# Optimization experiments

Hardware: AMD Instinct MI355X
Metric: run time of the kernel (lower is better)

## Reference

```python
import jax, jax.numpy as jnp
import numpy as np

# Tree/model constants (perfect binary plan tree in heap layout)
B = 256          # batch of plan trees
DEPTH = 10       # tree depth -> 512 leaves, 511 internal nodes
F = 64           # per-node feature dim
H = 512          # hidden_dim
DV = 64          # data_vec_dim
OUT = 1 + DV     # unit output: latency + data vector
N_LEAF = 2 ** (DEPTH - 1)
N_INT = N_LEAF - 1
N_NODE = N_INT + N_LEAF


def _mlp(x, w0, b0, w1, b1, w2, b2, wo, bo):
    # GenericUnit: num_layers=3 ReLU linears + linear head to OUT
    h = jax.nn.relu(x @ w0 + b0)
    h = jax.nn.relu(h @ w1 + b1)
    h = jax.nn.relu(h @ w2 + b2)
    return h @ wo + bo


def setup_inputs() -> dict:
    key = jax.random.key(0)
    ks = jax.random.split(key, 18)

    def lin(k, fan_in, shape):
        return (jax.random.normal(k, shape, jnp.float32) / np.sqrt(fan_in)).astype(jnp.float32)

    IIN = F + 2 * OUT  # internal unit input: features + two child outputs
    return {
        'leaf_feats': jax.random.normal(ks[0], (B, N_LEAF, F), jnp.float32),
        'internal_feats': jax.random.normal(ks[1], (B, N_INT, F), jnp.float32),
        # leaf unit (0 children)
        'lw0': lin(ks[2], F, (F, H)),   'lb0': jnp.zeros((H,), jnp.float32),
        'lw1': lin(ks[3], H, (H, H)),   'lb1': jnp.zeros((H,), jnp.float32),
        'lw2': lin(ks[4], H, (H, H)),   'lb2': jnp.zeros((H,), jnp.float32),
        'lwo': lin(ks[5], H, (H, OUT)), 'lbo': jnp.zeros((OUT,), jnp.float32),
        # internal unit (2 children)
        'iw0': lin(ks[6], IIN, (IIN, H)), 'ib0': jnp.zeros((H,), jnp.float32),
        'iw1': lin(ks[7], H, (H, H)),     'ib1': jnp.zeros((H,), jnp.float32),
        'iw2': lin(ks[8], H, (H, H)),     'ib2': jnp.zeros((H,), jnp.float32),
        'iwo': lin(ks[9], H, (H, OUT)),   'ibo': jnp.zeros((OUT,), jnp.float32),
    }


def reference(leaf_feats, internal_feats,
              lw0, lb0, lw1, lb1, lw2, lb2, lwo, lbo,
              iw0, ib0, iw1, ib1, iw2, ib2, iwo, ibo):
    # outputs buffer over all nodes, heap layout: internal [0, N_INT), leaves [N_INT, N_NODE)
    out = jnp.zeros((B, N_NODE, OUT), leaf_feats.dtype)
    out = out.at[:, N_INT:].set(_mlp(leaf_feats, lw0, lb0, lw1, lb1, lw2, lb2, lwo, lbo))
    # level-synchronous bottom-up over internal levels (fixed structural loop)
    for l in range(DEPTH - 2, -1, -1):
        s, e = 2 ** l - 1, 2 ** (l + 1) - 1
        left = out[:, 2 * s + 1:2 * e:2]        # children 2i+1
        right = out[:, 2 * s + 2:2 * e + 1:2]   # children 2i+2
        x = jnp.concatenate([internal_feats[:, s:e], left, right], axis=-1)
        out = out.at[:, s:e].set(_mlp(x, iw0, ib0, iw1, ib1, iw2, ib2, iwo, ibo))
    # root latency per tree: output[:, 0] of the root node
    return out[:, 0, 0]
```

## Files before the change

### kernel.cpp

```cpp
#include <hip/hip_runtime.h>
#include <cstdint>
#include <cstddef>
#include <type_traits>

#define OUT_DIM    65
#define TREE_STRIDE 66
#define N_NODE     1023
#define N_INTN     511

typedef _Float16 f16;
typedef _Float16 f16x8 __attribute__((ext_vector_type(8)));
typedef _Float16 f16x4 __attribute__((ext_vector_type(4)));
typedef float    f32x4 __attribute__((ext_vector_type(4)));

template<int V> using ic = std::integral_constant<int, V>;

#define MFMA(a, b, c) __builtin_amdgcn_mfma_f32_16x16x32_f16((a), (b), (c), 0, 0, 0)

template<int VM, int LG>
__device__ __forceinline__ void waitcnt_t() {
  asm volatile("s_waitcnt vmcnt(%0) lgkmcnt(%1)" :: "n"(VM), "n"(LG) : "memory");
}

template<int MT>
__device__ __forceinline__ void storeH_fn(f16* __restrict__ H, f32x4 (&acc)[MT][4],
                                          const float* __restrict__ bias,
                                          int wcb, int quad, int l16) {
#pragma unroll
  for (int mt = 0; mt < MT; mt++) {
#pragma unroll
    for (int nt = 0; nt < 4; nt++) {
      const int c0 = wcb + nt * 16 + quad * 4;
      const float4 bv = *(const float4*)(bias + c0);
      f16x4 hv;
      float v0 = acc[mt][nt][0] + bv.x; hv[0] = (f16)(v0 > 0.f ? v0 : 0.f);
      float v1 = acc[mt][nt][1] + bv.y; hv[1] = (f16)(v1 > 0.f ? v1 : 0.f);
      float v2 = acc[mt][nt][2] + bv.z; hv[2] = (f16)(v2 > 0.f ? v2 : 0.f);
      float v3 = acc[mt][nt][3] + bv.w; hv[3] = (f16)(v3 > 0.f ? v3 : 0.f);
      const int row = mt * 16 + l16;
      *(f16x4*)&H[row * 512 + (((c0 >> 3) ^ l16) << 3) + (quad & 1) * 4] = hv;
    }
  }
}

template<int NC, int MT, int NT, int BD, int AD, bool AGLOB, bool SWAP,
         typename GetB, typename GetA>
__device__ __forceinline__ void kloop(GetB getB, GetA getA, f32x4 (&acc)[MT][NT])
{
  f16x8 bs[BD][NT];
  f16x8 as[AD][MT];
#pragma unroll
  for (int c = 0; c < BD - 1 && c < NC; c++)
#pragma unroll
    for (int nt = 0; nt < NT; nt++) bs[c][nt] = getB(c, nt);
#pragma unroll
  for (int c = 0; c < AD - 1 && c < NC; c++)
#pragma unroll
    for (int mt = 0; mt < MT; mt++) as[c][mt] = getA(c, mt);

  auto lp = [&](auto&& self, auto Cc) -> void {
    constexpr int C = decltype(Cc)::value;
    if constexpr (C < NC) {
      if constexpr (C + BD - 1 < NC) {
#pragma unroll
        for (int nt = 0; nt < NT; nt++) bs[(C + BD - 1) % BD][nt] = getB(C + BD - 1, nt);
      }
      if constexpr (C + AD - 1 < NC) {
#pragma unroll
        for (int mt = 0; mt < MT; mt++) as[(C + AD - 1) % AD][mt] = getA(C + AD - 1, mt);
      }
      constexpr int BOUT = (BD - 1) < (NC - 1 - C) ? (BD - 1) : (NC - 1 - C);
      constexpr int AOUT = (AD - 1) < (NC - 1 - C) ? (AD - 1) : (NC - 1 - C);
      if constexpr (AGLOB) waitcnt_t<0, 0>();
      else                 waitcnt_t<NT * BOUT, MT * AOUT>();
      __builtin_amdgcn_s_setprio(1);
#pragma unroll
      for (int mt = 0; mt < MT; mt++)
#pragma unroll
        for (int nt = 0; nt < NT; nt++)
          acc[mt][nt] = SWAP ? MFMA(bs[C % BD][nt], as[C % AD][mt], acc[mt][nt])
                             : MFMA(as[C % AD][mt], bs[C % BD][nt], acc[mt][nt]);
      __builtin_amdgcn_s_setprio(0);
      self(self, ic<C + 1>{});
    }
  };
  lp(lp, ic<0>{});
}

template<int K, bool AGLOB, typename GetA>
__device__ __forceinline__ void run_layer(
    const f16* __restrict__ Wt, const float* __restrict__ bias,
    f16* __restrict__ H, int wave, int lane, int quad, int l16, GetA getA)
{
  constexpr int NC = K / 32;
  const int wcb = wave * 64;
  const f16* bbase = Wt + (long)(wave * 4) * 512 + lane * 8;
  auto getB = [&](int c, int nt) -> f16x8 {
    return *(const f16x8*)(bbase + (long)(c * 32 + nt) * 512);
  };
  f32x4 acc[4][4];
#pragma unroll
  for (int i = 0; i < 4; i++)
#pragma unroll
    for (int j = 0; j < 4; j++) acc[i][j] = f32x4{0.f, 0.f, 0.f, 0.f};

  kloop<NC, 4, 4, 4, 2, AGLOB, true>(getB, getA, acc);

  __syncthreads();
  storeH_fn<4>(H, acc, bias, wcb, quad, l16);
  __syncthreads();
}

__global__ __launch_bounds__(512, 2) void fused_mlp(
    const float* __restrict__ feats,
    const f16* __restrict__ w0t, const float* __restrict__ b0,
    const f16* __restrict__ w1t, const float* __restrict__ b1,
    const f16* __restrict__ w2t, const float* __restrict__ b2,
    const f16* __restrict__ wot, const float* __restrict__ bo,
    f16* __restrict__ tree, float* __restrict__ dOut, int lvl, int leaf)
{
  extern __shared__ f16 S[];
  f16* H = S;
  f16* X = S;

  const int tid  = threadIdx.x;
  const int wave = tid >> 6;
  const int lane = tid & 63;
  const int quad = lane >> 4;
  const int l16  = lane & 15;
  const long rowBase = (long)blockIdx.x * 64;

  if (!leaf) {
    for (int i = tid; i < 4096; i += 512) {
      int r = i >> 6, cc = i & 63;
      long rg = rowBase + r;
      long bbr = rg >> lvl;
      long ii = rg - (bbr << lvl);
      long nn = (1L << lvl) - 1 + ii;
      X[r * 232 + cc] = (f16)feats[(bbr * N_INTN + nn) * 64 + cc];
    }
    for (int i = tid; i < 4224; i += 512) {
      int r = i / 66, c = i - r * 66;
      long rg = rowBase + r;
      long bbr = rg >> lvl;
      long ii = rg - (bbr << lvl);
      long nn = (1L << lvl) - 1 + ii;
      const uint32_t* src = (const uint32_t*)(tree + (bbr * N_NODE + 2 * nn + 1) * TREE_STRIDE);
      *(uint32_t*)(X + r * 232 + 64 + 2 * c) = src[c];
    }
    for (int i = tid; i < 1792; i += 512) {
      int r = i / 28, cc = i - r * 28;
      X[r * 232 + 196 + cc] = (f16)0.f;
    }
    __syncthreads();
  }

  if (leaf) {
    auto gA = [&](int c, int mt) -> f16x8 {
      const float4* p = (const float4*)(feats + (rowBase + mt * 16 + l16) * 64 + c * 32 + quad * 8);
      float4 u0 = p[0], u1 = p[1];
      f16x8 a;
      a[0] = (f16)u0.x; a[1] = (f16)u0.y; a[2] = (f16)u0.z; a[3] = (f16)u0.w;
      a[4] = (f16)u1.x; a[5] = (f16)u1.y; a[6] = (f16)u1.z; a[7] = (f16)u1.w;
      return a;
    };
    run_layer<64, true>(w0t, b0, H, wave, lane, quad, l16, gA);
  } else {
    auto gA = [&](int c, int mt) -> f16x8 {
      int row = mt * 16 + l16;
      return *(const f16x8*)&X[row * 232 + c * 32 + quad * 8];
    };
    run_layer<224, false>(w0t, b0, H, wave, lane, quad, l16, gA);
  }

  auto getAH = [&](int c, int mt) -> f16x8 {
    int row = mt * 16 + l16;
    return *(const f16x8*)&H[row * 512 + ((((c * 4 + quad) ^ l16) << 3))];
  };
  run_layer<512, false>(w1t, b1, H, wave, lane, quad, l16, getAH);
  run_layer<512, false>(w2t, b2, H, wave, lane, quad, l16, getAH);

  if (wave < 4) {
    const f16* obase = wot + lane * 8;
    auto gB = [&](int c, int nt) -> f16x8 {
      return *(const f16x8*)(obase + (long)(c * 5 + nt) * 512);
    };
    const int orow = wave * 16 + l16;
    auto gA = [&](int c, int mt) -> f16x8 {
      return *(const f16x8*)&H[orow * 512 + ((((c * 4 + quad) ^ l16) << 3))];
    };
    f32x4 oacc[1][5];
#pragma unroll
    for (int i = 0; i < 5; i++) oacc[0][i] = f32x4{0.f, 0.f, 0.f, 0.f};

    kloop<16, 1, 5, 3, 2, false, false>(gB, gA, oacc);

#pragma unroll
    for (int nt = 0; nt < 5; nt++)
#pragma unroll
      for (int r = 0; r < 4; r++) {
        int col = nt * 16 + l16;
        long rg = rowBase + wave * 16 + quad * 4 + r;
        long b2_ = rg >> lvl;
        long ii  = rg - (b2_ << lvl);
        long node = (1L << lvl) - 1 + ii;
        if (col < OUT_DIM) {
          float v = oacc[0][nt][r] + bo[col];
          tree[(b2_ * N_NODE + node) * TREE_STRIDE + col] = (f16)v;
          if (lvl == 0 && col == 0) dOut[rg] = v;
        } else if (col == OUT_DIM) {
          tree[(b2_ * N_NODE + node) * TREE_STRIDE + col] = (f16)0.f;
        }
      }
  }
}

struct WSeg { const float* W; f16* Wt; int K, N, NB, hole, start; };
struct WPack { WSeg s[8]; int total; };

__global__ void wcast_all(WPack p) {
  int idx = blockIdx.x * 256 + threadIdx.x;
  if (idx >= p.total) return;
  int si = 0;
#pragma unroll
  for (int i = 1; i < 8; i++) if (idx >= p.s[i].start) si = i;
  WSeg sg = p.s[si];
  int e = idx - sg.start;
  int j = e & 7, lane = (e >> 3) & 63, q = e >> 9;
  int cb = q % sg.NB, c = q / sg.NB;
  int col = cb * 16 + (lane & 15);
  int k = c * 32 + (lane >> 4) * 8 + j;
  int srck = (k < sg.hole) ? k : k - 1;
  float v = (k != sg.hole && srck < sg.K && col < sg.N)
                ? sg.W[(long)srck * sg.N + col] : 0.f;
  sg.Wt[e] = (f16)v;
}

extern "C" void kernel_launch(void* const* d_in, const int* in_sizes, int n_in,
                              void* d_out, int out_size, void* d_ws, size_t ws_size,
                              hipStream_t stream) {
  const float* leaf_feats     = (const float*)d_in[0];
  const float* internal_feats = (const float*)d_in[1];
  const float* lw0 = (const float*)d_in[2];
  const float* lb0 = (const float*)d_in[3];
  const float* lw1 = (const float*)d_in[4];
  const float* lb1 = (const float*)d_in[5];
  const float* lw2 = (const float*)d_in[6];
  const float* lb2 = (const float*)d_in[7];
  const float* lwo = (const float*)d_in[8];
  const float* lbo = (const float*)d_in[9];
  const float* iw0 = (const float*)d_in[10];
  const float* ib0 = (const float*)d_in[11];
  const float* iw1 = (const float*)d_in[12];
  const float* ib1 = (const float*)d_in[13];
  const float* iw2 = (const float*)d_in[14];
  const float* ib2 = (const float*)d_in[15];
  const float* iwo = (const float*)d_in[16];
  const float* ibo = (const float*)d_in[17];
  float* dOut = (float*)d_out;

  char* ws = (char*)d_ws;
  size_t off = 0;
  auto alloc = [&](size_t bytes) -> void* {
    void* p = ws + off;
    off += (bytes + 255) & ~(size_t)255;
    return p;
  };

  f16* lw0t = (f16*)alloc((size_t)64  * 512 * 2);
  f16* lw1t = (f16*)alloc((size_t)512 * 512 * 2);
  f16* lw2t = (f16*)alloc((size_t)512 * 512 * 2);
  f16* lwot = (f16*)alloc((size_t)512 * 80  * 2);
  f16* iw0t = (f16*)alloc((size_t)224 * 512 * 2);
  f16* iw1t = (f16*)alloc((size_t)512 * 512 * 2);
  f16* iw2t = (f16*)alloc((size_t)512 * 512 * 2);
  f16* iwot = (f16*)alloc((size_t)512 * 80  * 2);
  f16* tree = (f16*)alloc((size_t)256 * N_NODE * TREE_STRIDE * 2);

  const int NOHOLE = 1 << 30;
  WPack p;
  int cum = 0;
  auto seg = [&](int i, const float* W, f16* Wt, int K, int N, int Kpad, int NB, int hole) {
    p.s[i] = {W, Wt, K, N, NB, hole, cum};
    cum += Kpad * NB * 16;
  };
  seg(0, lw0, lw0t, 64, 512, 64, 32, NOHOLE);
  seg(1, lw1, lw1t, 512, 512, 512, 32, NOHOLE);
  seg(2, lw2, lw2t, 512, 512, 512, 32, NOHOLE);
  seg(3, lwo, lwot, 512, 65, 512, 5, NOHOLE);
  seg(4, iw0, iw0t, 194, 512, 224, 32, 129);
  seg(5, iw1, iw1t, 512, 512, 512, 32, NOHOLE);
  seg(6, iw2, iw2t, 512, 512, 512, 32, NOHOLE);
  seg(7, iwo, iwot, 512, 65, 512, 5, NOHOLE);
  p.total = cum;
  wcast_all<<<dim3((cum + 255) / 256), dim3(256), 0, stream>>>(p);

  static bool attrSet = false;
  if (!attrSet) {
    hipFuncSetAttribute(reinterpret_cast<const void*>(fused_mlp),
                        hipFuncAttributeMaxDynamicSharedMemorySize, 65536);
    attrSet = true;
  }

  const size_t shmem = 65536;

  fused_mlp<<<dim3(2048), dim3(512), shmem, stream>>>(
      leaf_feats, lw0t, lb0, lw1t, lb1, lw2t, lb2, lwot, lbo, tree, dOut, 9, 1);

  for (int l = 8; l >= 0; l--) {
    fused_mlp<<<dim3(4u << l), dim3(512), shmem, stream>>>(
        internal_feats, iw0t, ib0, iw1t, ib1, iw2t, ib2, iwot, ibo, tree, dOut, l, 0);
  }

  (void)in_sizes; (void)n_in; (void)out_size; (void)ws_size;
}
```

Baseline: 662.2 us.

## Double rows per block to 128 so each weight tile serves more rows

Each block now processes 128 rows instead of 64, with 8 M-tiles per wave, which halves the number of blocks and doubles reuse of each loaded weight fragment. The leaf input is staged through shared memory rather than read directly from global, LDS grows to 128KB, and the software pipelining depth is reduced to make room for the larger accumulators. All 8 waves now compute the output head. The cost is more accumulator registers and LDS per block, which lowers occupancy, and fewer blocks at the small upper tree levels.

```diff
diff --git a/kernel.cpp b/kernel.cpp
--- a/kernel.cpp
+++ b/kernel.cpp
@@ -43,7 +43,7 @@
   }
 }
 
-template<int NC, int MT, int NT, int BD, int AD, bool AGLOB, bool SWAP,
+template<int NC, int MT, int NT, int BD, int AD, bool SWAP,
          typename GetB, typename GetA>
 __device__ __forceinline__ void kloop(GetB getB, GetA getA, f32x4 (&acc)[MT][NT])
 {
@@ -71,8 +71,7 @@
       }
       constexpr int BOUT = (BD - 1) < (NC - 1 - C) ? (BD - 1) : (NC - 1 - C);
       constexpr int AOUT = (AD - 1) < (NC - 1 - C) ? (AD - 1) : (NC - 1 - C);
-      if constexpr (AGLOB) waitcnt_t<0, 0>();
-      else                 waitcnt_t<NT * BOUT, MT * AOUT>();
+      waitcnt_t<NT * BOUT, MT * AOUT>();
       __builtin_amdgcn_s_setprio(1);
 #pragma unroll
       for (int mt = 0; mt < MT; mt++)
@@ -87,7 +86,7 @@
   lp(lp, ic<0>{});
 }
 
-template<int K, bool AGLOB, typename GetA>
+template<int K, typename GetA>
 __device__ __forceinline__ void run_layer(
     const f16* __restrict__ Wt, const float* __restrict__ bias,
     f16* __restrict__ H, int wave, int lane, int quad, int l16, GetA getA)
@@ -98,16 +97,16 @@
   auto getB = [&](int c, int nt) -> f16x8 {
     return *(const f16x8*)(bbase + (long)(c * 32 + nt) * 512);
   };
-  f32x4 acc[4][4];
-#pragma unroll
-  for (int i = 0; i < 4; i++)
+  f32x4 acc[8][4];
+#pragma unroll
+  for (int i = 0; i < 8; i++)
 #pragma unroll
     for (int j = 0; j < 4; j++) acc[i][j] = f32x4{0.f, 0.f, 0.f, 0.f};
 
-  kloop<NC, 4, 4, 4, 2, AGLOB, true>(getB, getA, acc);
+  kloop<NC, 8, 4, 2, 1, true>(getB, getA, acc);
 
   __syncthreads();
-  storeH_fn<4>(H, acc, bias, wcb, quad, l16);
+  storeH_fn<8>(H, acc, bias, wcb, quad, l16);
   __syncthreads();
 }
 
@@ -128,10 +127,16 @@
   const int lane = tid & 63;
   const int quad = lane >> 4;
   const int l16  = lane & 15;
-  const long rowBase = (long)blockIdx.x * 64;
-
-  if (!leaf) {
-    for (int i = tid; i < 4096; i += 512) {
+  const long rowBase = (long)blockIdx.x * 128;
+
+  if (leaf) {
+    for (int i = tid; i < 8192; i += 512) {
+      int r = i >> 6, cc = i & 63;
+      X[r * 72 + cc] = (f16)feats[(rowBase + r) * 64 + cc];
+    }
+    __syncthreads();
+  } else {
+    for (int i = tid; i < 8192; i += 512) {
       int r = i >> 6, cc = i & 63;
       long rg = rowBase + r;
       long bbr = rg >> lvl;
@@ -139,7 +144,7 @@
       long nn = (1L << lvl) - 1 + ii;
       X[r * 232 + cc] = (f16)feats[(bbr * N_INTN + nn) * 64 + cc];
     }
-    for (int i = tid; i < 4224; i += 512) {
+    for (int i = tid; i < 8448; i += 512) {
       int r = i / 66, c = i - r * 66;
       long rg = rowBase + r;
       long bbr = rg >> lvl;
@@ -148,7 +153,7 @@
       const uint32_t* src = (const uint32_t*)(tree + (bbr * N_NODE + 2 * nn + 1) * TREE_STRIDE);
       *(uint32_t*)(X + r * 232 + 64 + 2 * c) = src[c];
     }
-    for (int i = tid; i < 1792; i += 512) {
+    for (int i = tid; i < 3584; i += 512) {
       int r = i / 28, cc = i - r * 28;
       X[r * 232 + 196 + cc] = (f16)0.f;
     }
@@ -157,30 +162,26 @@
 
   if (leaf) {
     auto gA = [&](int c, int mt) -> f16x8 {
-      const float4* p = (const float4*)(feats + (rowBase + mt * 16 + l16) * 64 + c * 32 + quad * 8);
-      float4 u0 = p[0], u1 = p[1];
-      f16x8 a;
-      a[0] = (f16)u0.x; a[1] = (f16)u0.y; a[2] = (f16)u0.z; a[3] = (f16)u0.w;
-      a[4] = (f16)u1.x; a[5] = (f16)u1.y; a[6] = (f16)u1.z; a[7] = (f16)u1.w;
-      return a;
+      int row = mt * 16 + l16;
+      return *(const f16x8*)&X[row * 72 + c * 32 + quad * 8];
     };
-    run_layer<64, true>(w0t, b0, H, wave, lane, quad, l16, gA);
+    run_layer<64>(w0t, b0, H, wave, lane, quad, l16, gA);
   } else {
     auto gA = [&](int c, int mt) -> f16x8 {
       int row = mt * 16 + l16;
       return *(const f16x8*)&X[row * 232 + c * 32 + quad * 8];
     };
-    run_layer<224, false>(w0t, b0, H, wave, lane, quad, l16, gA);
+    run_layer<224>(w0t, b0, H, wave, lane, quad, l16, gA);
   }
 
   auto getAH = [&](int c, int mt) -> f16x8 {
     int row = mt * 16 + l16;
     return *(const f16x8*)&H[row * 512 + ((((c * 4 + quad) ^ l16) << 3))];
   };
-  run_layer<512, false>(w1t, b1, H, wave, lane, quad, l16, getAH);
-  run_layer<512, false>(w2t, b2, H, wave, lane, quad, l16, getAH);
-
-  if (wave < 4) {
+  run_layer<512>(w1t, b1, H, wave, lane, quad, l16, getAH);
+  run_layer<512>(w2t, b2, H, wave, lane, quad, l16, getAH);
+
+  {
     const f16* obase = wot + lane * 8;
     auto gB = [&](int c, int nt) -> f16x8 {
       return *(const f16x8*)(obase + (long)(c * 5 + nt) * 512);
@@ -193,7 +194,7 @@
 #pragma unroll
     for (int i = 0; i < 5; i++) oacc[0][i] = f32x4{0.f, 0.f, 0.f, 0.f};
 
-    kloop<16, 1, 5, 3, 2, false, false>(gB, gA, oacc);
+    kloop<16, 1, 5, 2, 1, false>(gB, gA, oacc);
 
 #pragma unroll
     for (int nt = 0; nt < 5; nt++)
@@ -298,17 +299,17 @@
   static bool attrSet = false;
   if (!attrSet) {
     hipFuncSetAttribute(reinterpret_cast<const void*>(fused_mlp),
-                        hipFuncAttributeMaxDynamicSharedMemorySize, 65536);
+                        hipFuncAttributeMaxDynamicSharedMemorySize, 131072);
     attrSet = true;
   }
 
-  const size_t shmem = 65536;
-
-  fused_mlp<<<dim3(2048), dim3(512), shmem, stream>>>(
+  const size_t shmem = 131072;
+
+  fused_mlp<<<dim3(1024), dim3(512), shmem, stream>>>(
       leaf_feats, lw0t, lb0, lw1t, lb1, lw2t, lb2, lwot, lbo, tree, dOut, 9, 1);
 
   for (int l = 8; l >= 0; l--) {
-    fused_mlp<<<dim3(4u << l), dim3(512), shmem, stream>>>(
+    fused_mlp<<<dim3(2u << l), dim3(512), shmem, stream>>>(
         internal_feats, iw0t, ib0, iw1t, ib1, iw2t, ib2, iwot, ibo, tree, dOut, l, 0);
   }
 
```

Measured after the change: 1.002 ms. +51.4%, slower.

## Fuse the last six tree levels into one per-tree persistent tail kernel

Applied to the files above, without the earlier changes.

Tree levels 5 through 0 are now handled by a single tail_mlp kernel with one block per tree. Each block walks those levels internally, keeping child outputs in shared-memory ping-pong buffers and running a 32-row (MT=2) MLP tile. This replaces six small kernel launches, each with few blocks, and the global round-trips through the tree buffer between levels. In exchange the upper levels compute on padded 32-row tiles when fewer nodes exist, and only 256 blocks run.

```diff
diff --git a/kernel.cpp b/kernel.cpp
--- a/kernel.cpp
+++ b/kernel.cpp
@@ -87,7 +87,7 @@
   lp(lp, ic<0>{});
 }
 
-template<int K, bool AGLOB, typename GetA>
+template<int K, int MT, bool AGLOB, typename GetA>
 __device__ __forceinline__ void run_layer(
     const f16* __restrict__ Wt, const float* __restrict__ bias,
     f16* __restrict__ H, int wave, int lane, int quad, int l16, GetA getA)
@@ -98,16 +98,16 @@
   auto getB = [&](int c, int nt) -> f16x8 {
     return *(const f16x8*)(bbase + (long)(c * 32 + nt) * 512);
   };
-  f32x4 acc[4][4];
-#pragma unroll
-  for (int i = 0; i < 4; i++)
+  f32x4 acc[MT][4];
+#pragma unroll
+  for (int i = 0; i < MT; i++)
 #pragma unroll
     for (int j = 0; j < 4; j++) acc[i][j] = f32x4{0.f, 0.f, 0.f, 0.f};
 
-  kloop<NC, 4, 4, 4, 2, AGLOB, true>(getB, getA, acc);
+  kloop<NC, MT, 4, 4, 2, AGLOB, true>(getB, getA, acc);
 
   __syncthreads();
-  storeH_fn<4>(H, acc, bias, wcb, quad, l16);
+  storeH_fn<MT>(H, acc, bias, wcb, quad, l16);
   __syncthreads();
 }
 
@@ -164,21 +164,21 @@
       a[4] = (f16)u1.x; a[5] = (f16)u1.y; a[6] = (f16)u1.z; a[7] = (f16)u1.w;
       return a;
     };
-    run_layer<64, true>(w0t, b0, H, wave, lane, quad, l16, gA);
+    run_layer<64, 4, true>(w0t, b0, H, wave, lane, quad, l16, gA);
   } else {
     auto gA = [&](int c, int mt) -> f16x8 {
       int row = mt * 16 + l16;
       return *(const f16x8*)&X[row * 232 + c * 32 + quad * 8];
     };
-    run_layer<224, false>(w0t, b0, H, wave, lane, quad, l16, gA);
+    run_layer<224, 4, false>(w0t, b0, H, wave, lane, quad, l16, gA);
   }
 
   auto getAH = [&](int c, int mt) -> f16x8 {
     int row = mt * 16 + l16;
     return *(const f16x8*)&H[row * 512 + ((((c * 4 + quad) ^ l16) << 3))];
   };
-  run_layer<512, false>(w1t, b1, H, wave, lane, quad, l16, getAH);
-  run_layer<512, false>(w2t, b2, H, wave, lane, quad, l16, getAH);
+  run_layer<512, 4, false>(w1t, b1, H, wave, lane, quad, l16, getAH);
+  run_layer<512, 4, false>(w2t, b2, H, wave, lane, quad, l16, getAH);
 
   if (wave < 4) {
     const f16* obase = wot + lane * 8;
@@ -212,6 +212,111 @@
           tree[(b2_ * N_NODE + node) * TREE_STRIDE + col] = (f16)0.f;
         }
       }
+  }
+}
+
+__global__ __launch_bounds__(512, 2) void tail_mlp(
+    const float* __restrict__ feats,
+    const f16* __restrict__ w0t, const float* __restrict__ b0,
+    const f16* __restrict__ w1t, const float* __restrict__ b1,
+    const f16* __restrict__ w2t, const float* __restrict__ b2,
+    const f16* __restrict__ wot, const float* __restrict__ bo,
+    const f16* __restrict__ tree, float* __restrict__ dOut)
+{
+  extern __shared__ f16 S[];
+  f16* H = S;
+  f16* X = S;
+  f16* childA = S + 16384;
+  f16* childB = S + 18496;
+
+  const long b   = blockIdx.x;
+  const int tid  = threadIdx.x;
+  const int wave = tid >> 6;
+  const int lane = tid & 63;
+  const int quad = lane >> 4;
+  const int l16  = lane & 15;
+
+  f16* prev = childA;
+  f16* cur  = childB;
+
+  auto getAH = [&](int c, int mt) -> f16x8 {
+    int row = mt * 16 + l16;
+    return *(const f16x8*)&H[row * 512 + ((((c * 4 + quad) ^ l16) << 3))];
+  };
+  auto gAX = [&](int c, int mt) -> f16x8 {
+    int row = mt * 16 + l16;
+    return *(const f16x8*)&X[row * 232 + c * 32 + quad * 8];
+  };
+
+  for (int l = 5; l >= 0; --l) {
+    const int M = 1 << l;
+
+    {
+      const int r  = tid >> 4;
+      const int p  = tid & 15;
+      const int rr = r < M ? r : M - 1;
+      const long nn = (long)(M - 1) + rr;
+      const float* fsrc = feats + (b * N_INTN + nn) * 64 + p * 4;
+      f16* xr = X + r * 232;
+      float4 v = *(const float4*)fsrc;
+      f16x4 h; h[0] = (f16)v.x; h[1] = (f16)v.y; h[2] = (f16)v.z; h[3] = (f16)v.w;
+      *(f16x4*)(xr + p * 4) = h;
+      const uint32_t* csrc = (l == 5)
+          ? (const uint32_t*)(tree + (b * N_NODE + 2 * nn + 1) * TREE_STRIDE)
+          : (const uint32_t*)(prev + 2 * rr * 66);
+      uint32_t* xd = (uint32_t*)(xr + 64);
+#pragma unroll
+      for (int j = 0; j < 5; j++) {
+        int c = p * 5 + j;
+        if (c < 66) xd[c] = csrc[c];
+      }
+#pragma unroll
+      for (int j = 0; j < 2; j++) {
+        int z = p * 2 + j;
+        if (z < 28) xr[196 + z] = (f16)0.f;
+      }
+      __syncthreads();
+    }
+
+    run_layer<224, 2, false>(w0t, b0, H, wave, lane, quad, l16, gAX);
+    run_layer<512, 2, false>(w1t, b1, H, wave, lane, quad, l16, getAH);
+    run_layer<512, 2, false>(w2t, b2, H, wave, lane, quad, l16, getAH);
+
+    if (wave < 2) {
+      const f16* obase = wot + lane * 8;
+      auto gB = [&](int c, int nt) -> f16x8 {
+        return *(const f16x8*)(obase + (long)(c * 5 + nt) * 512);
+      };
+      const int orow = wave * 16 + l16;
+      auto gA = [&](int c, int mt) -> f16x8 {
+        return *(const f16x8*)&H[orow * 512 + ((((c * 4 + quad) ^ l16) << 3))];
+      };
+      f32x4 oacc[1][5];
+#pragma unroll
+      for (int i = 0; i < 5; i++) oacc[0][i] = f32x4{0.f, 0.f, 0.f, 0.f};
+
+      kloop<16, 1, 5, 3, 2, false, false>(gB, gA, oacc);
+
+      const int rowb = wave * 16 + quad * 4;
+#pragma unroll
+      for (int nt = 0; nt < 5; nt++)
+#pragma unroll
+        for (int r = 0; r < 4; r++) {
+          int col = nt * 16 + l16;
+          int row = rowb + r;
+          if (row < M) {
+            if (col < OUT_DIM) {
+              float v = oacc[0][nt][r] + bo[col];
+              cur[row * 66 + col] = (f16)v;
+              if (l == 0 && col == 0 && row == 0) dOut[b] = v;
+            } else if (col == OUT_DIM) {
+              cur[row * 66 + col] = (f16)0.f;
+            }
+          }
+        }
+    }
+    __syncthreads();
+    f16* t = prev; prev = cur; cur = t;
   }
 }
 
@@ -299,18 +404,24 @@
   if (!attrSet) {
     hipFuncSetAttribute(reinterpret_cast<const void*>(fused_mlp),
                         hipFuncAttributeMaxDynamicSharedMemorySize, 65536);
+    hipFuncSetAttribute(reinterpret_cast<const void*>(tail_mlp),
+                        hipFuncAttributeMaxDynamicSharedMemorySize, 41216);
     attrSet = true;
   }
 
-  const size_t shmem = 65536;
+  const size_t shmem     = 65536;
+  const size_t tailShmem = 41216;
 
   fused_mlp<<<dim3(2048), dim3(512), shmem, stream>>>(
       leaf_feats, lw0t, lb0, lw1t, lb1, lw2t, lb2, lwot, lbo, tree, dOut, 9, 1);
 
-  for (int l = 8; l >= 0; l--) {
+  for (int l = 8; l >= 6; l--) {
     fused_mlp<<<dim3(4u << l), dim3(512), shmem, stream>>>(
         internal_feats, iw0t, ib0, iw1t, ib1, iw2t, ib2, iwot, ibo, tree, dOut, l, 0);
   }
 
+  tail_mlp<<<dim3(256), dim3(512), tailShmem, stream>>>(
+      internal_feats, iw0t, ib0, iw1t, ib1, iw2t, ib2, iwot, ibo, tree, dOut);
+
   (void)in_sizes; (void)n_in; (void)out_size; (void)ws_size;
 }
```

Result: slower. 1.044 ms (+57.7%).
